# Optimization experiments

Measured on AMD Instinct MI355X. Metric: run time of the kernel, lower is better.

The kernel has to match this reference:

```python
import jax, jax.numpy as jnp
import numpy as np


def _gru_layer(x, w_ih, w_hh, b_ih, b_hh):
    """PyTorch-semantics GRU over x:[B,T,I]. w_ih:[3H,I], w_hh:[3H,H]."""
    B, T, I = x.shape
    H = w_hh.shape[1]
    # precompute input-side gates for all timesteps: [T,B,3H]
    gx = (jnp.einsum('bti,gi->btg', x, w_ih) + b_ih).transpose(1, 0, 2)

    def step(h, gx_t):
        gh = h @ w_hh.T + b_hh  # [B,3H]
        xr, xz, xn = jnp.split(gx_t, 3, axis=-1)
        hr, hz, hn = jnp.split(gh, 3, axis=-1)
        r = jax.nn.sigmoid(xr + hr)
        z = jax.nn.sigmoid(xz + hz)
        n = jnp.tanh(xn + r * hn)
        h_new = (1.0 - z) * n + z * h
        return h_new, h_new

    h0 = jnp.zeros((B, H), dtype=x.dtype)
    _, hs = jax.lax.scan(step, h0, gx)  # hs: [T,B,H]
    return hs.transpose(1, 0, 2)


def _gru_params(key, in_size, hidden):
    k = 1.0 / np.sqrt(hidden)
    k1, k2, k3, k4 = jax.random.split(key, 4)
    w_ih = jax.random.uniform(k1, (3 * hidden, in_size), minval=-k, maxval=k, dtype=jnp.float32)
    w_hh = jax.random.uniform(k2, (3 * hidden, hidden), minval=-k, maxval=k, dtype=jnp.float32)
    b_ih = jax.random.uniform(k3, (3 * hidden,), minval=-k, maxval=k, dtype=jnp.float32)
    b_hh = jax.random.uniform(k4, (3 * hidden,), minval=-k, maxval=k, dtype=jnp.float32)
    return w_ih, w_hh, b_ih, b_hh


def setup_inputs() -> dict:
    key = jax.random.key(0)
    ks = jax.random.split(key, 6)
    B, T = 256, 1024
    x = jax.random.normal(ks[0], (B, T), dtype=jnp.float32)
    sizes = [(1, 256), (256, 128), (128, 128), (128, 256)]
    d = {'x': x}
    for i, (isz, h) in enumerate(sizes):
        w_ih, w_hh, b_ih, b_hh = _gru_params(ks[1 + i], isz, h)
        d[f'w_ih{i+1}'] = w_ih
        d[f'w_hh{i+1}'] = w_hh
        d[f'b_ih{i+1}'] = b_ih
        d[f'b_hh{i+1}'] = b_hh
    kw, kb = jax.random.split(ks[5])
    kk = 1.0 / np.sqrt(256.0)
    d['w_out'] = jax.random.uniform(kw, (1, 256), minval=-kk, maxval=kk, dtype=jnp.float32)
    d['b_out'] = jax.random.uniform(kb, (1,), minval=-kk, maxval=kk, dtype=jnp.float32)
    return d


def reference(x, w_ih1, w_hh1, b_ih1, b_hh1,
              w_ih2, w_hh2, b_ih2, b_hh2,
              w_ih3, w_hh3, b_ih3, b_hh3,
              w_ih4, w_hh4, b_ih4, b_hh4,
              w_out, b_out):
    h = x[..., None]  # [B,T,1]
    h = _gru_layer(h, w_ih1, w_hh1, b_ih1, b_hh1)
    h = _gru_layer(h, w_ih2, w_hh2, b_ih2, b_hh2)
    h = _gru_layer(h, w_ih3, w_hh3, b_ih3, b_hh3)
    h = _gru_layer(h, w_ih4, w_hh4, b_ih4, b_hh4)
    y = jnp.einsum('bth,oh->bto', h, w_out) + b_out  # TimeDistributed Linear(256,1)
    return y.reshape(y.shape[0], -1)  # flatten from dim 1 -> [B,T]
```

## Files before the change

kernel.cpp:

```cpp
#include <hip/hip_runtime.h>
#include <math.h>


__device__ __forceinline__ float sigmoidf_(float v) {
    return 1.0f / (1.0f + __expf(-v));
}

__global__ void prep_k(const float* __restrict__ src, float* __restrict__ dst,
                       int H, int J) {
    int idx = blockIdx.x * 256 + threadIdx.x;
    int total = 3 * H * J;
    if (idx < total) {
        int g = idx / (H * J);
        int rem = idx - g * H * J;
        int u = rem / J;
        int j = rem - u * J;
        dst[(u * 3 + g) * J + j] = src[(g * H + u) * J + j];
    }
}


__device__ __forceinline__ void flag_st(int* p, int v) {
    __hip_atomic_store(p, v, __ATOMIC_RELAXED, __HIP_MEMORY_SCOPE_AGENT);
}
__device__ __forceinline__ int flag_ld(const int* p) {
    return __hip_atomic_load(p, __ATOMIC_RELAXED, __HIP_MEMORY_SCOPE_AGENT);
}
__device__ __forceinline__ void ex_store(float* p, float v) {
    __hip_atomic_store(p, v, __ATOMIC_RELAXED, __HIP_MEMORY_SCOPE_AGENT);
}

__device__ __forceinline__ void pollwait(const int* p, int tgt, bool active) {
    if (threadIdx.x < 64) {
        int spins = 0;
        while (true) {
            int v = active ? flag_ld(p) : 0x7fffffff;
            if (__all(v >= tgt)) break;
            if (++spins > 200000) break;
            __builtin_amdgcn_s_sleep(1);
        }
    }
    __syncthreads();
}

template <int J>
__device__ __forceinline__ void stageX(float* dst, const float* src) {
    constexpr int NF4 = (32 * J) / 1024;
    constexpr int LJ = (J == 256) ? 8 : 7;
    float4 tmp[NF4];
    #pragma unroll
    for (int k = 0; k < NF4; ++k) {
        const float* p = src + (size_t)(k * 256 + threadIdx.x) * 4;
        asm volatile("global_load_dwordx4 %0, %1, off sc0 sc1"
                     : "=v"(tmp[k]) : "v"(p) : "memory");
    }
    asm volatile("s_waitcnt vmcnt(0)" ::: "memory");
    #pragma unroll
    for (int k = 0; k < NF4; ++k) {
        int i = (k * 256 + threadIdx.x) * 4;
        int b = i >> LJ;
        int j = i & (J - 1);
        *(float4*)(dst + b * (J + 4) + j) = tmp[k];
    }
}

template <int J>
__device__ __forceinline__ void zero32(float* dst) {
    for (int i = threadIdx.x; i < 32 * (J + 4); i += 256) dst[i] = 0.0f;
}

template <int KB, int J>
__device__ __forceinline__ void dot3(const float* __restrict__ w3,
                                     const float* __restrict__ hst, int b0,
                                     float* ar, float* az, float* ac) {
    const float4* wr = (const float4*)w3;
    const float4* wz = (const float4*)(w3 + J);
    const float4* wn = (const float4*)(w3 + 2 * J);
    const float* rows[KB];
    #pragma unroll
    for (int k = 0; k < KB; ++k) rows[k] = hst + (b0 + k * (32 / KB)) * (J + 4);
    #pragma unroll 4
    for (int j4 = 0; j4 < J / 4; ++j4) {
        float4 a = wr[j4];
        float4 c = wz[j4];
        float4 d = wn[j4];
        #pragma unroll
        for (int k = 0; k < KB; ++k) {
            float4 hv = *(const float4*)(rows[k] + j4 * 4);
            ar[k] = fmaf(hv.x, a.x, ar[k]); ar[k] = fmaf(hv.y, a.y, ar[k]);
            ar[k] = fmaf(hv.z, a.z, ar[k]); ar[k] = fmaf(hv.w, a.w, ar[k]);
            az[k] = fmaf(hv.x, c.x, az[k]); az[k] = fmaf(hv.y, c.y, az[k]);
            az[k] = fmaf(hv.z, c.z, az[k]); az[k] = fmaf(hv.w, c.w, az[k]);
            ac[k] = fmaf(hv.x, d.x, ac[k]); ac[k] = fmaf(hv.y, d.y, ac[k]);
            ac[k] = fmaf(hv.z, d.z, ac[k]); ac[k] = fmaf(hv.w, d.w, ac[k]);
        }
    }
}

__global__ __launch_bounds__(256) void gru_pipe_kernel(
    const float* __restrict__ x,
    const float* __restrict__ w_ih1,
    const float* __restrict__ b_ih1, const float* __restrict__ b_hh1,
    const float* __restrict__ b_ih2, const float* __restrict__ b_hh2,
    const float* __restrict__ b_ih3, const float* __restrict__ b_hh3,
    const float* __restrict__ b_ih4, const float* __restrict__ b_hh4,
    const float* __restrict__ wA_hh1,
    const float* __restrict__ wA_ih2,
    const float* __restrict__ wA_hh2,
    const float* __restrict__ wA_ih3,
    const float* __restrict__ wA_hh3,
    const float* __restrict__ wA_ih4,
    const float* __restrict__ wA_hh4,
    const float* __restrict__ w_out, const float* __restrict__ b_out,
    int* __restrict__ flags,
    float* __restrict__ ex,
    float* __restrict__ out)
{
    const int tid = threadIdx.x;
    extern __shared__ float smem[];
    __shared__ float xs[32];
    __shared__ float wsum[4][4][8];

    const int bg = blockIdx.x & 7;
    const int rest = blockIdx.x >> 3;
    const int s = rest >> 3;
    const int us = rest & 7;

    int* fb = flags + bg * 128;
    int* arr_own = fb + s * 32;

    const int* pT = arr_own; int dT = -1000000000; bool aT = false;
    const int* pM = arr_own; int dM = -1000000000; bool aM = false;
    if (tid < 8) {
        if (s > 0) { pT = fb + (s - 1) * 32 + tid; dT = 1; aT = true; }
        pM = arr_own + tid; dM = 0; aM = true;
    } else if (tid < 16) {
        if (s < 3) { pT = fb + (s + 1) * 32 + (tid - 8); dT = -3; aT = true; }
    }

    float* exb = ex + (size_t)bg * 98304;
    float* h1r = exb;
    float* h2r = exb + 32768;
    float* h3r = exb + 49152;
    float* h4r = exb + 65536;

    if (s == 0) {
        float* wlds = smem;
        float* hprev = smem + 24704;
        {
            const float* srcw = wA_hh1 + (size_t)us * 32 * 768;
            for (int i = tid; i < 24576; i += 256) {
                int uu = i / 768, r = i - uu * 768;
                wlds[uu * 772 + r] = srcw[i];
            }
        }
        __syncthreads();
        const int ul = tid >> 3, b0 = tid & 7;
        const int u = us * 32 + ul;
        const float* wh = wlds + ul * 772;
        const float br = b_ih1[u] + b_hh1[u];
        const float bz = b_ih1[u + 256] + b_hh1[u + 256];
        const float bxn = b_ih1[u + 512];
        const float bhn = b_hh1[u + 512];
        const float wir = w_ih1[u], wiz = w_ih1[u + 256], win = w_ih1[u + 512];
        for (int t = 0; t < 1024; ++t) {
            pollwait(pT, t + dT, aT);
            if (tid < 32) xs[tid] = x[(size_t)(bg * 32 + tid) * 1024 + t];
            pollwait(pM, t + dM, aM);
            if (t > 0) stageX<256>(hprev, h1r + (size_t)((t - 1) & 3) * 8192);
            else       zero32<256>(hprev);
            __syncthreads();
            float ar[4], az[4], axn[4], ahn[4];
            #pragma unroll
            for (int k = 0; k < 4; ++k) {
                float xv = xs[b0 + 8 * k];
                ar[k] = br + xv * wir; az[k] = bz + xv * wiz;
                axn[k] = bxn + xv * win; ahn[k] = bhn;
            }
            dot3<4, 256>(wh, hprev, b0, ar, az, ahn);
            float* hout = h1r + (size_t)(t & 3) * 8192;
            #pragma unroll
            for (int k = 0; k < 4; ++k) {
                int b = b0 + 8 * k;
                float hp = hprev[b * 260 + u];
                float r = sigmoidf_(ar[k]);
                float z = sigmoidf_(az[k]);
                float n = tanhf(axn[k] + r * ahn[k]);
                ex_store(hout + b * 256 + u, (1.f - z) * n + z * hp);
            }
            asm volatile("s_waitcnt vmcnt(0)" ::: "memory");
            __syncthreads();
            if (tid == 0) flag_st(arr_own + us, t + 1);
        }
    } else if (s == 1) {
        float* wlds = smem;
        float* hin = smem + 6208;
        float* hprev = smem + 14528;
        {
            const float* srcw = wA_hh2 + (size_t)us * 16 * 384;
            for (int i = tid; i < 6144; i += 256) {
                int uu = i / 384, r = i - uu * 384;
                wlds[uu * 388 + r] = srcw[i];
            }
        }
        __syncthreads();
        const int ul = tid >> 4, b0 = tid & 15;
        const int u = us * 16 + ul;
        const float* wi = wA_ih2 + (size_t)u * 768;
        const float* wh = wlds + ul * 388;
        const float br = b_ih2[u] + b_hh2[u];
        const float bz = b_ih2[u + 128] + b_hh2[u + 128];
        const float bxn = b_ih2[u + 256];
        const float bhn = b_hh2[u + 256];
        for (int t = 0; t < 1024; ++t) {
            pollwait(pT, t + dT, aT);
            stageX<256>(hin, h1r + (size_t)(t & 3) * 8192);
            __syncthreads();
            float ar[2] = {br, br}, az[2] = {bz, bz};
            float axn[2] = {bxn, bxn}, ahn[2] = {bhn, bhn};
            dot3<2, 256>(wi, hin, b0, ar, az, axn);
            pollwait(pM, t + dM, aM);
            if (t > 0) stageX<128>(hprev, h2r + (size_t)((t - 1) & 3) * 4096);
            else       zero32<128>(hprev);
            __syncthreads();
            dot3<2, 128>(wh, hprev, b0, ar, az, ahn);
            float* hout = h2r + (size_t)(t & 3) * 4096;
            #pragma unroll
            for (int k = 0; k < 2; ++k) {
                int b = b0 + 16 * k;
                float hp = hprev[b * 132 + u];
                float r = sigmoidf_(ar[k]);
                float z = sigmoidf_(az[k]);
                float n = tanhf(axn[k] + r * ahn[k]);
                ex_store(hout + b * 128 + u, (1.f - z) * n + z * hp);
            }
            asm volatile("s_waitcnt vmcnt(0)" ::: "memory");
            __syncthreads();
            if (tid == 0) flag_st(arr_own + us, t + 1);
        }
    } else if (s == 2) {
        float* wlds = smem;
        float* hin = smem + 6208;
        float* hprev = smem + 10432;
        {
            const float* srcw = wA_hh3 + (size_t)us * 16 * 384;
            for (int i = tid; i < 6144; i += 256) {
                int uu = i / 384, r = i - uu * 384;
                wlds[uu * 388 + r] = srcw[i];
            }
        }
        __syncthreads();
        const int ul = tid >> 4, b0 = tid & 15;
        const int u = us * 16 + ul;
        const float* wi = wA_ih3 + (size_t)u * 384;
        const float* wh = wlds + ul * 388;
        const float br = b_ih3[u] + b_hh3[u];
        const float bz = b_ih3[u + 128] + b_hh3[u + 128];
        const float bxn = b_ih3[u + 256];
        const float bhn = b_hh3[u + 256];
        for (int t = 0; t < 1024; ++t) {
            pollwait(pT, t + dT, aT);
            stageX<128>(hin, h2r + (size_t)(t & 3) * 4096);
            __syncthreads();
            float ar[2] = {br, br}, az[2] = {bz, bz};
            float axn[2] = {bxn, bxn}, ahn[2] = {bhn, bhn};
            dot3<2, 128>(wi, hin, b0, ar, az, axn);
            pollwait(pM, t + dM, aM);
            if (t > 0) stageX<128>(hprev, h3r + (size_t)((t - 1) & 3) * 4096);
            else       zero32<128>(hprev);
            __syncthreads();
            dot3<2, 128>(wh, hprev, b0, ar, az, ahn);
            float* hout = h3r + (size_t)(t & 3) * 4096;
            #pragma unroll
            for (int k = 0; k < 2; ++k) {
                int b = b0 + 16 * k;
                float hp = hprev[b * 132 + u];
                float r = sigmoidf_(ar[k]);
                float z = sigmoidf_(az[k]);
                float n = tanhf(axn[k] + r * ahn[k]);
                ex_store(hout + b * 128 + u, (1.f - z) * n + z * hp);
            }
            asm volatile("s_waitcnt vmcnt(0)" ::: "memory");
            __syncthreads();
            if (tid == 0) flag_st(arr_own + us, t + 1);
        }
    } else {
        float* wlds = smem;
        float* hin = smem + 24704;
        float* hprev = smem + 28928;
        {
            const float* srcw = wA_hh4 + (size_t)us * 32 * 768;
            for (int i = tid; i < 24576; i += 256) {
                int uu = i / 768, r = i - uu * 768;
                wlds[uu * 772 + r] = srcw[i];
            }
        }
        __syncthreads();
        const int ul = tid >> 3, b0 = tid & 7;
        const int u = us * 32 + ul;
        const float* wi = wA_ih4 + (size_t)u * 384;
        const float* wh = wlds + ul * 772;
        const float br = b_ih4[u] + b_hh4[u];
        const float bz = b_ih4[u + 256] + b_hh4[u + 256];
        const float bxn = b_ih4[u + 512];
        const float bhn = b_hh4[u + 512];
        const float wo = w_out[u];
        for (int t = 0; t < 1024; ++t) {
            pollwait(pT, t + dT, aT);
            stageX<128>(hin, h3r + (size_t)(t & 3) * 4096);
            __syncthreads();
            float ar[4], az[4], axn[4], ahn[4];
            #pragma unroll
            for (int k = 0; k < 4; ++k) {
                ar[k] = br; az[k] = bz; axn[k] = bxn; ahn[k] = bhn;
            }
            dot3<4, 128>(wi, hin, b0, ar, az, axn);
            pollwait(pM, t + dM, aM);
            if (t > 0) stageX<256>(hprev, h4r + (size_t)((t - 1) & 3) * 8192);
            else       zero32<256>(hprev);
            __syncthreads();
            dot3<4, 256>(wh, hprev, b0, ar, az, ahn);
            float* hout = h4r + (size_t)(t & 3) * 8192;
            float pk[4];
            #pragma unroll
            for (int k = 0; k < 4; ++k) {
                int b = b0 + 8 * k;
                float hp = hprev[b * 260 + u];
                float r = sigmoidf_(ar[k]);
                float z = sigmoidf_(az[k]);
                float n = tanhf(axn[k] + r * ahn[k]);
                float hnew = (1.f - z) * n + z * hp;
                ex_store(hout + b * 256 + u, hnew);
                pk[k] = wo * hnew;
            }
            #pragma unroll
            for (int k = 0; k < 4; ++k) {
                pk[k] += __shfl_xor(pk[k], 8, 64);
                pk[k] += __shfl_xor(pk[k], 16, 64);
                pk[k] += __shfl_xor(pk[k], 32, 64);
            }
            if ((tid & 63) < 8) {
                int w = tid >> 6;
                #pragma unroll
                for (int k = 0; k < 4; ++k) wsum[w][k][tid & 7] = pk[k];
            }
            asm volatile("s_waitcnt vmcnt(0)" ::: "memory");
            __syncthreads();
            if (tid == 0) flag_st(arr_own + us, t + 1);
            if (tid < 32) {
                int k = tid >> 3, bb = tid & 7;
                float ssum = wsum[0][k][bb] + wsum[1][k][bb] +
                             wsum[2][k][bb] + wsum[3][k][bb];
                if (us == 0) ssum += b_out[0];
                atomicAdd(out + (size_t)(bg * 32 + bb + 8 * k) * 1024 + t, ssum);
            }
        }
    }
}

extern "C" void kernel_launch(void* const* d_in, const int* in_sizes, int n_in,
                              void* d_out, int out_size, void* d_ws, size_t ws_size,
                              hipStream_t stream) {
    const float* x     = (const float*)d_in[0];
    const float* w_ih1 = (const float*)d_in[1];
    const float* w_hh1 = (const float*)d_in[2];
    const float* b_ih1 = (const float*)d_in[3];
    const float* b_hh1 = (const float*)d_in[4];
    const float* w_ih2 = (const float*)d_in[5];
    const float* w_hh2 = (const float*)d_in[6];
    const float* b_ih2 = (const float*)d_in[7];
    const float* b_hh2 = (const float*)d_in[8];
    const float* w_ih3 = (const float*)d_in[9];
    const float* w_hh3 = (const float*)d_in[10];
    const float* b_ih3 = (const float*)d_in[11];
    const float* b_hh3 = (const float*)d_in[12];
    const float* w_ih4 = (const float*)d_in[13];
    const float* w_hh4 = (const float*)d_in[14];
    const float* b_ih4 = (const float*)d_in[15];
    const float* b_hh4 = (const float*)d_in[16];
    const float* w_out = (const float*)d_in[17];
    const float* b_out = (const float*)d_in[18];

    float* ws = (float*)d_ws;
    float* wA_hh1 = ws;
    float* wA_ih2 = wA_hh1 + 196608;
    float* wA_hh2 = wA_ih2 + 98304;
    float* wA_ih3 = wA_hh2 + 49152;
    float* wA_hh3 = wA_ih3 + 49152;
    float* wA_ih4 = wA_hh3 + 49152;
    float* wA_hh4 = wA_ih4 + 98304;
    float* ex     = wA_hh4 + 196608;
    int*   flags  = (int*)(ex + 786432);

    hipMemsetAsync(flags, 0, 1024 * sizeof(int), stream);
    hipMemsetAsync(d_out, 0, 256 * 1024 * sizeof(float), stream);

    prep_k<<<768, 256, 0, stream>>>(w_hh1, wA_hh1, 256, 256);
    prep_k<<<384, 256, 0, stream>>>(w_ih2, wA_ih2, 128, 256);
    prep_k<<<192, 256, 0, stream>>>(w_hh2, wA_hh2, 128, 128);
    prep_k<<<192, 256, 0, stream>>>(w_ih3, wA_ih3, 128, 128);
    prep_k<<<192, 256, 0, stream>>>(w_hh3, wA_hh3, 128, 128);
    prep_k<<<384, 256, 0, stream>>>(w_ih4, wA_ih4, 256, 128);
    prep_k<<<768, 256, 0, stream>>>(w_hh4, wA_hh4, 256, 256);

    const int dyn_lds = 37248 * (int)sizeof(float);
    (void)hipFuncSetAttribute((const void*)gru_pipe_kernel,
                              hipFuncAttributeMaxDynamicSharedMemorySize, dyn_lds);

    gru_pipe_kernel<<<256, 256, dyn_lds, stream>>>(
        x, w_ih1, b_ih1, b_hh1, b_ih2, b_hh2, b_ih3, b_hh3, b_ih4, b_hh4,
        wA_hh1, wA_ih2, wA_hh2, wA_ih3, wA_hh3, wA_ih4, wA_hh4,
        w_out, b_out, flags, ex, (float*)d_out);
}
```

Measured before the change: 18.27 ms.

## Prefetch next-step inputs, coalesce ring stores via LDS, and lighten flag polling

The persistent pipelined GRU kernel now polls flags per wavefront with cached flag values, so each wave skips the poll once the target is already met, and the trailing barrier after polling is removed. Layers 2-4 speculatively prefetch the next timestep's input hidden state into registers when the upstream flag already allows it, overlapping that load with the gate math. Each layer's output is staged in LDS and written to the global ring with coalesced stores instead of scattered per-thread stores. tanhf is replaced by an exp-based approximation. The cost is extra LDS, an extra barrier per step and more registers, and removing the barrier after polling makes the synchronisation more delicate.

After: 19.55 ms. +7.0%, slower.

```diff
diff --git a/kernel.cpp b/kernel.cpp
--- a/kernel.cpp
+++ b/kernel.cpp
@@ -4,6 +4,10 @@
 
 __device__ __forceinline__ float sigmoidf_(float v) {
     return 1.0f / (1.0f + __expf(-v));
+}
+__device__ __forceinline__ float tanhf_(float v) {
+    float e = __expf(2.0f * v);
+    return 1.0f - 2.0f / (e + 1.0f);
 }
 
 __global__ void prep_k(const float* __restrict__ src, float* __restrict__ dst,
@@ -30,43 +34,67 @@
     __hip_atomic_store(p, v, __ATOMIC_RELAXED, __HIP_MEMORY_SCOPE_AGENT);
 }
 
-__device__ __forceinline__ void pollwait(const int* p, int tgt, bool active) {
-    if (threadIdx.x < 64) {
-        int spins = 0;
-        while (true) {
-            int v = active ? flag_ld(p) : 0x7fffffff;
-            if (__all(v >= tgt)) break;
-            if (++spins > 200000) break;
-            __builtin_amdgcn_s_sleep(1);
-        }
-    }
-    __syncthreads();
-}
+__device__ __forceinline__ void pollw(const int* p, int tgt, bool active,
+                                      int& fc) {
+    bool need = active && (fc < tgt);
+    if (!__any(need)) return;
+    int spins = 0;
+    while (true) {
+        if (need) { fc = flag_ld(p); need = (fc < tgt); }
+        if (!__any(need)) return;
+        if (++spins > 16) __builtin_amdgcn_s_sleep(1);
+        if (spins > 200000) return;
+    }
+}
+
 
 template <int J>
-__device__ __forceinline__ void stageX(float* dst, const float* src) {
+__device__ __forceinline__ void stage_load(float4* r, const float* src) {
     constexpr int NF4 = (32 * J) / 1024;
-    constexpr int LJ = (J == 256) ? 8 : 7;
-    float4 tmp[NF4];
     #pragma unroll
     for (int k = 0; k < NF4; ++k) {
         const float* p = src + (size_t)(k * 256 + threadIdx.x) * 4;
         asm volatile("global_load_dwordx4 %0, %1, off sc0 sc1"
-                     : "=v"(tmp[k]) : "v"(p) : "memory");
-    }
-    asm volatile("s_waitcnt vmcnt(0)" ::: "memory");
+                     : "=v"(r[k]) : "v"(p) : "memory");
+    }
+}
+
+template <int J>
+__device__ __forceinline__ void stage_write(const float4* r, float* dst) {
+    constexpr int NF4 = (32 * J) / 1024;
+    constexpr int LJ = (J == 256) ? 8 : 7;
     #pragma unroll
     for (int k = 0; k < NF4; ++k) {
         int i = (k * 256 + threadIdx.x) * 4;
         int b = i >> LJ;
         int j = i & (J - 1);
-        *(float4*)(dst + b * (J + 4) + j) = tmp[k];
-    }
+        *(float4*)(dst + b * (J + 4) + j) = r[k];
+    }
+}
+
+template <int J>
+__device__ __forceinline__ void stageX(float* dst, const float* src) {
+    float4 tmp[(32 * J) / 1024];
+    stage_load<J>(tmp, src);
+    asm volatile("s_waitcnt vmcnt(0)" ::: "memory");
+    stage_write<J>(tmp, dst);
 }
 
 template <int J>
 __device__ __forceinline__ void zero32(float* dst) {
     for (int i = threadIdx.x; i < 32 * (J + 4); i += 256) dst[i] = 0.0f;
+}
+
+template <int U, int J>
+__device__ __forceinline__ void ring_store(float* hout, const float* hst) {
+    constexpr int LU = (U == 32) ? 5 : 4;
+    #pragma unroll
+    for (int k = 0; k < (32 * U) / 256; ++k) {
+        int i = k * 256 + threadIdx.x;
+        int b = i >> LU;
+        int c = i & (U - 1);
+        ex_store(hout + b * J + c, hst[b * (U + 4) + c]);
+    }
 }
 
 template <int KB, int J>
@@ -117,6 +145,7 @@
     float* __restrict__ out)
 {
     const int tid = threadIdx.x;
+    const int lane = tid & 63;
     extern __shared__ float smem[];
     __shared__ float xs[32];
     __shared__ float wsum[4][4][8];
@@ -129,14 +158,16 @@
     int* fb = flags + bg * 128;
     int* arr_own = fb + s * 32;
 
-    const int* pT = arr_own; int dT = -1000000000; bool aT = false;
-    const int* pM = arr_own; int dM = -1000000000; bool aM = false;
-    if (tid < 8) {
-        if (s > 0) { pT = fb + (s - 1) * 32 + tid; dT = 1; aT = true; }
-        pM = arr_own + tid; dM = 0; aM = true;
-    } else if (tid < 16) {
-        if (s < 3) { pT = fb + (s + 1) * 32 + (tid - 8); dT = -3; aT = true; }
-    }
+    const int* pT = arr_own; int dT = 0; bool aT = false;
+    const int* pM = arr_own; bool aM = false;
+    if (lane < 8) {
+        if (s > 0) { pT = fb + (s - 1) * 32 + lane; dT = 1; aT = true; }
+        pM = arr_own + lane; aM = true;
+    } else if (lane < 16) {
+        if (s < 3) { pT = fb + (s + 1) * 32 + (lane - 8); dT = -3; aT = true; }
+    }
+    const bool aUp = (s > 0) && (lane < 8);
+    int fcT = 0, fcM = 0;
 
     float* exb = ex + (size_t)bg * 98304;
     float* h1r = exb;
@@ -147,6 +178,7 @@
     if (s == 0) {
         float* wlds = smem;
         float* hprev = smem + 24704;
+        float* hst = smem + 33024;
         {
             const float* srcw = wA_hh1 + (size_t)us * 32 * 768;
             for (int i = tid; i < 24576; i += 256) {
@@ -164,9 +196,9 @@
         const float bhn = b_hh1[u + 512];
         const float wir = w_ih1[u], wiz = w_ih1[u + 256], win = w_ih1[u + 512];
         for (int t = 0; t < 1024; ++t) {
-            pollwait(pT, t + dT, aT);
+            pollw(pT, t + dT, aT, fcT);
             if (tid < 32) xs[tid] = x[(size_t)(bg * 32 + tid) * 1024 + t];
-            pollwait(pM, t + dM, aM);
+            pollw(pM, t, aM, fcM);
             if (t > 0) stageX<256>(hprev, h1r + (size_t)((t - 1) & 3) * 8192);
             else       zero32<256>(hprev);
             __syncthreads();
@@ -185,9 +217,11 @@
                 float hp = hprev[b * 260 + u];
                 float r = sigmoidf_(ar[k]);
                 float z = sigmoidf_(az[k]);
-                float n = tanhf(axn[k] + r * ahn[k]);
-                ex_store(hout + b * 256 + u, (1.f - z) * n + z * hp);
-            }
+                float n = tanhf_(axn[k] + r * ahn[k]);
+                hst[b * 36 + ul] = (1.f - z) * n + z * hp;
+            }
+            __syncthreads();
+            ring_store<32, 256>(hout + us * 32, hst);
             asm volatile("s_waitcnt vmcnt(0)" ::: "memory");
             __syncthreads();
             if (tid == 0) flag_st(arr_own + us, t + 1);
@@ -196,6 +230,7 @@
         float* wlds = smem;
         float* hin = smem + 6208;
         float* hprev = smem + 14528;
+        float* hst = smem + 18752;
         {
             const float* srcw = wA_hh2 + (size_t)us * 16 * 384;
             for (int i = tid; i < 6144; i += 256) {
@@ -212,18 +247,27 @@
         const float bz = b_ih2[u + 128] + b_hh2[u + 128];
         const float bxn = b_ih2[u + 256];
         const float bhn = b_hh2[u + 256];
+        float4 pregs[8];
+        bool pf = false;
         for (int t = 0; t < 1024; ++t) {
-            pollwait(pT, t + dT, aT);
-            stageX<256>(hin, h1r + (size_t)(t & 3) * 8192);
+            pollw(pT, t + dT, aT && (lane >= 8 || !pf), fcT);
+            if (pf) stage_write<256>(pregs, hin);
+            else    stageX<256>(hin, h1r + (size_t)(t & 3) * 8192);
             __syncthreads();
             float ar[2] = {br, br}, az[2] = {bz, bz};
             float axn[2] = {bxn, bxn}, ahn[2] = {bhn, bhn};
             dot3<2, 256>(wi, hin, b0, ar, az, axn);
-            pollwait(pM, t + dM, aM);
+            pollw(pM, t, aM, fcM);
             if (t > 0) stageX<128>(hprev, h2r + (size_t)((t - 1) & 3) * 4096);
             else       zero32<128>(hprev);
             __syncthreads();
             dot3<2, 128>(wh, hprev, b0, ar, az, ahn);
+            pf = false;
+            if (t < 1023) {
+                if (aUp && fcT < t + 2) fcT = flag_ld(pT);
+                pf = __all(!aUp || fcT >= t + 2);
+                if (pf) stage_load<256>(pregs, h1r + (size_t)((t + 1) & 3) * 8192);
+            }
             float* hout = h2r + (size_t)(t & 3) * 4096;
             #pragma unroll
             for (int k = 0; k < 2; ++k) {
@@ -231,9 +275,11 @@
                 float hp = hprev[b * 132 + u];
                 float r = sigmoidf_(ar[k]);
                 float z = sigmoidf_(az[k]);
-                float n = tanhf(axn[k] + r * ahn[k]);
-                ex_store(hout + b * 128 + u, (1.f - z) * n + z * hp);
-            }
+                float n = tanhf_(axn[k] + r * ahn[k]);
+                hst[b * 20 + ul] = (1.f - z) * n + z * hp;
+            }
+            __syncthreads();
+            ring_store<16, 128>(hout + us * 16, hst);
             asm volatile("s_waitcnt vmcnt(0)" ::: "memory");
             __syncthreads();
             if (tid == 0) flag_st(arr_own + us, t + 1);
@@ -242,6 +288,7 @@
         float* wlds = smem;
         float* hin = smem + 6208;
         float* hprev = smem + 10432;
+        float* hst = smem + 14656;
         {
             const float* srcw = wA_hh3 + (size_t)us * 16 * 384;
             for (int i = tid; i < 6144; i += 256) {
@@ -258,18 +305,27 @@
         const float bz = b_ih3[u + 128] + b_hh3[u + 128];
         const float bxn = b_ih3[u + 256];
         const float bhn = b_hh3[u + 256];
+        float4 pregs[4];
+        bool pf = false;
         for (int t = 0; t < 1024; ++t) {
-            pollwait(pT, t + dT, aT);
-            stageX<128>(hin, h2r + (size_t)(t & 3) * 4096);
+            pollw(pT, t + dT, aT && (lane >= 8 || !pf), fcT);
+            if (pf) stage_write<128>(pregs, hin);
+            else    stageX<128>(hin, h2r + (size_t)(t & 3) * 4096);
             __syncthreads();
             float ar[2] = {br, br}, az[2] = {bz, bz};
             float axn[2] = {bxn, bxn}, ahn[2] = {bhn, bhn};
             dot3<2, 128>(wi, hin, b0, ar, az, axn);
-            pollwait(pM, t + dM, aM);
+            pollw(pM, t, aM, fcM);
             if (t > 0) stageX<128>(hprev, h3r + (size_t)((t - 1) & 3) * 4096);
             else       zero32<128>(hprev);
             __syncthreads();
             dot3<2, 128>(wh, hprev, b0, ar, az, ahn);
+            pf = false;
+            if (t < 1023) {
+                if (aUp && fcT < t + 2) fcT = flag_ld(pT);
+                pf = __all(!aUp || fcT >= t + 2);
+                if (pf) stage_load<128>(pregs, h2r + (size_t)((t + 1) & 3) * 4096);
+            }
             float* hout = h3r + (size_t)(t & 3) * 4096;
             #pragma unroll
             for (int k = 0; k < 2; ++k) {
@@ -277,9 +333,11 @@
                 float hp = hprev[b * 132 + u];
                 float r = sigmoidf_(ar[k]);
                 float z = sigmoidf_(az[k]);
-                float n = tanhf(axn[k] + r * ahn[k]);
-                ex_store(hout + b * 128 + u, (1.f - z) * n + z * hp);
-            }
+                float n = tanhf_(axn[k] + r * ahn[k]);
+                hst[b * 20 + ul] = (1.f - z) * n + z * hp;
+            }
+            __syncthreads();
+            ring_store<16, 128>(hout + us * 16, hst);
             asm volatile("s_waitcnt vmcnt(0)" ::: "memory");
             __syncthreads();
             if (tid == 0) flag_st(arr_own + us, t + 1);
@@ -288,6 +346,7 @@
         float* wlds = smem;
         float* hin = smem + 24704;
         float* hprev = smem + 28928;
+        float* hst = smem + 37248;
         {
             const float* srcw = wA_hh4 + (size_t)us * 32 * 768;
             for (int i = tid; i < 24576; i += 256) {
@@ -305,9 +364,12 @@
         const float bxn = b_ih4[u + 512];
         const float bhn = b_hh4[u + 512];
         const float wo = w_out[u];
+        float4 pregs[4];
+        bool pf = false;
         for (int t = 0; t < 1024; ++t) {
-            pollwait(pT, t + dT, aT);
-            stageX<128>(hin, h3r + (size_t)(t & 3) * 4096);
+            pollw(pT, t + dT, aT && !pf, fcT);
+            if (pf) stage_write<128>(pregs, hin);
+            else    stageX<128>(hin, h3r + (size_t)(t & 3) * 4096);
             __syncthreads();
             float ar[4], az[4], axn[4], ahn[4];
             #pragma unroll
@@ -315,11 +377,17 @@
                 ar[k] = br; az[k] = bz; axn[k] = bxn; ahn[k] = bhn;
             }
             dot3<4, 128>(wi, hin, b0, ar, az, axn);
-            pollwait(pM, t + dM, aM);
+            pollw(pM, t, aM, fcM);
             if (t > 0) stageX<256>(hprev, h4r + (size_t)((t - 1) & 3) * 8192);
             else       zero32<256>(hprev);
             __syncthreads();
             dot3<4, 256>(wh, hprev, b0, ar, az, ahn);
+            pf = false;
+            if (t < 1023) {
+                if (aUp && fcT < t + 2) fcT = flag_ld(pT);
+                pf = __all(!aUp || fcT >= t + 2);
+                if (pf) stage_load<128>(pregs, h3r + (size_t)((t + 1) & 3) * 4096);
+            }
             float* hout = h4r + (size_t)(t & 3) * 8192;
             float pk[4];
             #pragma unroll
@@ -328,9 +396,9 @@
                 float hp = hprev[b * 260 + u];
                 float r = sigmoidf_(ar[k]);
                 float z = sigmoidf_(az[k]);
-                float n = tanhf(axn[k] + r * ahn[k]);
+                float n = tanhf_(axn[k] + r * ahn[k]);
                 float hnew = (1.f - z) * n + z * hp;
-                ex_store(hout + b * 256 + u, hnew);
+                hst[b * 36 + ul] = hnew;
                 pk[k] = wo * hnew;
             }
             #pragma unroll
@@ -344,6 +412,8 @@
                 #pragma unroll
                 for (int k = 0; k < 4; ++k) wsum[w][k][tid & 7] = pk[k];
             }
+            __syncthreads();
+            ring_store<32, 256>(hout + us * 32, hst);
             asm volatile("s_waitcnt vmcnt(0)" ::: "memory");
             __syncthreads();
             if (tid == 0) flag_st(arr_own + us, t + 1);
@@ -392,8 +462,8 @@
     float* ex     = wA_hh4 + 196608;
     int*   flags  = (int*)(ex + 786432);
 
-    hipMemsetAsync(flags, 0, 1024 * sizeof(int), stream);
-    hipMemsetAsync(d_out, 0, 256 * 1024 * sizeof(float), stream);
+    (void)hipMemsetAsync(flags, 0, 1024 * sizeof(int), stream);
+    (void)hipMemsetAsync(d_out, 0, 256 * 1024 * sizeof(float), stream);
 
     prep_k<<<768, 256, 0, stream>>>(w_hh1, wA_hh1, 256, 256);
     prep_k<<<384, 256, 0, stream>>>(w_ih2, wA_ih2, 128, 256);
@@ -403,7 +473,7 @@
     prep_k<<<384, 256, 0, stream>>>(w_ih4, wA_ih4, 256, 128);
     prep_k<<<768, 256, 0, stream>>>(w_hh4, wA_hh4, 256, 256);
 
-    const int dyn_lds = 37248 * (int)sizeof(float);
+    const int dyn_lds = 38400 * (int)sizeof(float);
     (void)hipFuncSetAttribute((const void*)gru_pipe_kernel,
                               hipFuncAttributeMaxDynamicSharedMemorySize, dyn_lds);
 
```

## Restructure GRU recurrent matvecs with per-wave batch tiles and shuffle reduce-scatter

Applied to the files above, without the earlier changes.

Each wave now stages only its own 8-batch slice of the hidden state, so the block-wide barrier before each matvec goes away. Lanes split the reduction dimension across 8 lanes and combine partial sums with a shuffle-based reduce-scatter. Results are staged in LDS and written to the ring buffer with coalesced stores. A cheaper exp-based tanh replaces tanhf, and flag polling caches the last observed value so it can skip redundant loads. The cost is more register pressure from large accumulator arrays, extra shuffle work, and a small change in tanh accuracy.

Result: slower. 19.65 ms (+7.5%).

```diff
diff --git a/kernel.cpp b/kernel.cpp
--- a/kernel.cpp
+++ b/kernel.cpp
@@ -4,6 +4,10 @@
 
 __device__ __forceinline__ float sigmoidf_(float v) {
     return 1.0f / (1.0f + __expf(-v));
+}
+__device__ __forceinline__ float tanhf_(float v) {
+    float e = __expf(2.0f * v);
+    return 1.0f - 2.0f / (e + 1.0f);
 }
 
 __global__ void prep_k(const float* __restrict__ src, float* __restrict__ dst,
@@ -30,69 +34,135 @@
     __hip_atomic_store(p, v, __ATOMIC_RELAXED, __HIP_MEMORY_SCOPE_AGENT);
 }
 
-__device__ __forceinline__ void pollwait(const int* p, int tgt, bool active) {
+__device__ __forceinline__ void pollwait(const int* p, int tgt, bool active,
+                                         int& fc) {
     if (threadIdx.x < 64) {
-        int spins = 0;
-        while (true) {
-            int v = active ? flag_ld(p) : 0x7fffffff;
-            if (__all(v >= tgt)) break;
-            if (++spins > 200000) break;
-            __builtin_amdgcn_s_sleep(1);
+        bool need = active && (fc < tgt);
+        if (__any(need)) {
+            int spins = 0;
+            while (true) {
+                if (need) { fc = flag_ld(p); need = (fc < tgt); }
+                if (!__any(need)) break;
+                if (++spins > 200000) break;
+                __builtin_amdgcn_s_sleep(1);
+            }
         }
     }
     __syncthreads();
 }
 
+
 template <int J>
-__device__ __forceinline__ void stageX(float* dst, const float* src) {
-    constexpr int NF4 = (32 * J) / 1024;
-    constexpr int LJ = (J == 256) ? 8 : 7;
+__device__ __forceinline__ void stageW(float* dst, const float* src) {
+    constexpr int NF4 = J / 32;
+    const int lane = threadIdx.x & 63;
     float4 tmp[NF4];
     #pragma unroll
     for (int k = 0; k < NF4; ++k) {
-        const float* p = src + (size_t)(k * 256 + threadIdx.x) * 4;
+        const float* p = src + (size_t)(k * 64 + lane) * 4;
         asm volatile("global_load_dwordx4 %0, %1, off sc0 sc1"
                      : "=v"(tmp[k]) : "v"(p) : "memory");
     }
     asm volatile("s_waitcnt vmcnt(0)" ::: "memory");
     #pragma unroll
-    for (int k = 0; k < NF4; ++k) {
-        int i = (k * 256 + threadIdx.x) * 4;
-        int b = i >> LJ;
-        int j = i & (J - 1);
-        *(float4*)(dst + b * (J + 4) + j) = tmp[k];
-    }
+    for (int k = 0; k < NF4; ++k)
+        *(float4*)(dst + (k * 64 + lane) * 4) = tmp[k];
 }
 
 template <int J>
-__device__ __forceinline__ void zero32(float* dst) {
-    for (int i = threadIdx.x; i < 32 * (J + 4); i += 256) dst[i] = 0.0f;
-}
-
-template <int KB, int J>
-__device__ __forceinline__ void dot3(const float* __restrict__ w3,
-                                     const float* __restrict__ hst, int b0,
-                                     float* ar, float* az, float* ac) {
-    const float4* wr = (const float4*)w3;
-    const float4* wz = (const float4*)(w3 + J);
-    const float4* wn = (const float4*)(w3 + 2 * J);
-    const float* rows[KB];
+__device__ __forceinline__ void zeroW(float* dst) {
+    const int lane = threadIdx.x & 63;
     #pragma unroll
-    for (int k = 0; k < KB; ++k) rows[k] = hst + (b0 + k * (32 / KB)) * (J + 4);
-    #pragma unroll 4
-    for (int j4 = 0; j4 < J / 4; ++j4) {
-        float4 a = wr[j4];
-        float4 c = wz[j4];
-        float4 d = wn[j4];
+    for (int k = 0; k < J / 32; ++k)
+        *(float4*)(dst + (k * 64 + lane) * 4) = make_float4(0.f, 0.f, 0.f, 0.f);
+}
+
+template <int U, int J>
+__device__ __forceinline__ void ring_store(float* hout, const float* hst) {
+    constexpr int LU = (U == 32) ? 5 : 4;
+    #pragma unroll
+    for (int k = 0; k < (32 * U) / 256; ++k) {
+        int i = k * 256 + threadIdx.x;
+        int b = i >> LU;
+        int c = i & (U - 1);
+        ex_store(hout + b * J + c, hst[b * (U + 4) + c]);
+    }
+}
+
+
+template <int J, int WST>
+__device__ __forceinline__ void dotA4(const float* __restrict__ wb,
+                                      const float* __restrict__ hb, int kl,
+                                      float (&a)[8][12]) {
+    #pragma unroll 2
+    for (int it = 0; it < J / 32; ++it) {
+        const int j = (it * 8 + kl) * 4;
+        float4 h4[8];
         #pragma unroll
-        for (int k = 0; k < KB; ++k) {
-            float4 hv = *(const float4*)(rows[k] + j4 * 4);
-            ar[k] = fmaf(hv.x, a.x, ar[k]); ar[k] = fmaf(hv.y, a.y, ar[k]);
-            ar[k] = fmaf(hv.z, a.z, ar[k]); ar[k] = fmaf(hv.w, a.w, ar[k]);
-            az[k] = fmaf(hv.x, c.x, az[k]); az[k] = fmaf(hv.y, c.y, az[k]);
-            az[k] = fmaf(hv.z, c.z, az[k]); az[k] = fmaf(hv.w, c.w, az[k]);
-            ac[k] = fmaf(hv.x, d.x, ac[k]); ac[k] = fmaf(hv.y, d.y, ac[k]);
-            ac[k] = fmaf(hv.z, d.z, ac[k]); ac[k] = fmaf(hv.w, d.w, ac[k]);
+        for (int b = 0; b < 8; ++b)
+            h4[b] = *(const float4*)(hb + b * J + j);
+        #pragma unroll
+        for (int i = 0; i < 4; ++i) {
+            #pragma unroll
+            for (int ch = 0; ch < 3; ++ch) {
+                float4 w = *(const float4*)(wb + i * WST + ch * J + j);
+                #pragma unroll
+                for (int b8 = 0; b8 < 8; ++b8) {
+                    float& acc = a[i * 2 + (b8 >> 2)][ch * 4 + (b8 & 3)];
+                    acc = fmaf(w.x, h4[b8].x, acc);
+                    acc = fmaf(w.y, h4[b8].y, acc);
+                    acc = fmaf(w.z, h4[b8].z, acc);
+                    acc = fmaf(w.w, h4[b8].w, acc);
+                }
+            }
+        }
+    }
+}
+
+template <int J, int WST>
+__device__ __forceinline__ void dotB2(const float* __restrict__ wb,
+                                      const float* __restrict__ hb, int kl,
+                                      float (&a)[8][6]) {
+    #pragma unroll 2
+    for (int it = 0; it < J / 32; ++it) {
+        const int j = (it * 8 + kl) * 4;
+        float4 h4[8];
+        #pragma unroll
+        for (int b = 0; b < 8; ++b)
+            h4[b] = *(const float4*)(hb + b * J + j);
+        #pragma unroll
+        for (int i = 0; i < 2; ++i) {
+            #pragma unroll
+            for (int ch = 0; ch < 3; ++ch) {
+                float4 w = *(const float4*)(wb + i * WST + ch * J + j);
+                #pragma unroll
+                for (int b8 = 0; b8 < 8; ++b8) {
+                    float& acc = a[i * 4 + (b8 >> 1)][ch * 2 + (b8 & 1)];
+                    acc = fmaf(w.x, h4[b8].x, acc);
+                    acc = fmaf(w.y, h4[b8].y, acc);
+                    acc = fmaf(w.z, h4[b8].z, acc);
+                    acc = fmaf(w.w, h4[b8].w, acc);
+                }
+            }
+        }
+    }
+}
+
+template <int G, int F>
+__device__ __forceinline__ void rscat(float (&a)[G][F], int kl) {
+    #pragma unroll
+    for (int lev = 0; (1 << lev) < G; ++lev) {
+        const int m = 1 << lev;
+        const int g = G >> (lev + 1);
+        const bool hi = ((kl >> lev) & 1) != 0;
+        #pragma unroll
+        for (int gg = 0; gg < g; ++gg) {
+            #pragma unroll
+            for (int f = 0; f < F; ++f) {
+                float give = hi ? a[gg][f] : a[gg + g][f];
+                float got = __shfl_xor(give, m, 64);
+                a[gg][f] = (hi ? a[gg + g][f] : a[gg][f]) + got;
+            }
         }
     }
 }
@@ -117,9 +187,13 @@
     float* __restrict__ out)
 {
     const int tid = threadIdx.x;
+    const int lane = tid & 63;
+    const int w = tid >> 6;
+    const int usl = lane >> 3;
+    const int kl = lane & 7;
+    const int gf = ((kl & 1) << 2) | (kl & 2) | ((kl >> 2) & 1);
     extern __shared__ float smem[];
     __shared__ float xs[32];
-    __shared__ float wsum[4][4][8];
 
     const int bg = blockIdx.x & 7;
     const int rest = blockIdx.x >> 3;
@@ -130,13 +204,14 @@
     int* arr_own = fb + s * 32;
 
     const int* pT = arr_own; int dT = -1000000000; bool aT = false;
-    const int* pM = arr_own; int dM = -1000000000; bool aM = false;
+    const int* pM = arr_own; bool aM = false;
     if (tid < 8) {
         if (s > 0) { pT = fb + (s - 1) * 32 + tid; dT = 1; aT = true; }
-        pM = arr_own + tid; dM = 0; aM = true;
+        pM = arr_own + tid; aM = true;
     } else if (tid < 16) {
         if (s < 3) { pT = fb + (s + 1) * 32 + (tid - 8); dT = -3; aT = true; }
     }
+    int fcT = 0, fcM = 0;
 
     float* exb = ex + (size_t)bg * 98304;
     float* h1r = exb;
@@ -147,6 +222,7 @@
     if (s == 0) {
         float* wlds = smem;
         float* hprev = smem + 24704;
+        float* hst = smem + 32896;
         {
             const float* srcw = wA_hh1 + (size_t)us * 32 * 768;
             for (int i = tid; i < 24576; i += 256) {
@@ -155,39 +231,39 @@
             }
         }
         __syncthreads();
-        const int ul = tid >> 3, b0 = tid & 7;
-        const int u = us * 32 + ul;
-        const float* wh = wlds + ul * 772;
+        const int u_sl = usl * 4 + (gf >> 1);
+        const int bhi = gf & 1;
+        const int u = us * 32 + u_sl;
+        const float* wbh = wlds + usl * 4 * 772;
+        const float* hbh = hprev + w * 2048;
         const float br = b_ih1[u] + b_hh1[u];
         const float bz = b_ih1[u + 256] + b_hh1[u + 256];
         const float bxn = b_ih1[u + 512];
         const float bhn = b_hh1[u + 512];
         const float wir = w_ih1[u], wiz = w_ih1[u + 256], win = w_ih1[u + 512];
         for (int t = 0; t < 1024; ++t) {
-            pollwait(pT, t + dT, aT);
+            pollwait(pT, t + dT, aT, fcT);
             if (tid < 32) xs[tid] = x[(size_t)(bg * 32 + tid) * 1024 + t];
-            pollwait(pM, t + dM, aM);
-            if (t > 0) stageX<256>(hprev, h1r + (size_t)((t - 1) & 3) * 8192);
-            else       zero32<256>(hprev);
-            __syncthreads();
-            float ar[4], az[4], axn[4], ahn[4];
-            #pragma unroll
-            for (int k = 0; k < 4; ++k) {
-                float xv = xs[b0 + 8 * k];
-                ar[k] = br + xv * wir; az[k] = bz + xv * wiz;
-                axn[k] = bxn + xv * win; ahn[k] = bhn;
-            }
-            dot3<4, 256>(wh, hprev, b0, ar, az, ahn);
+            pollwait(pM, t, aM, fcM);
+            if (t > 0) stageW<256>(hprev + w * 2048,
+                                   h1r + (size_t)((t - 1) & 3) * 8192 + w * 2048);
+            else       zeroW<256>(hprev + w * 2048);
+            float ah[8][12] = {};
+            dotA4<256, 772>(wbh, hbh, kl, ah);
+            rscat<8, 12>(ah, kl);
             float* hout = h1r + (size_t)(t & 3) * 8192;
             #pragma unroll
-            for (int k = 0; k < 4; ++k) {
-                int b = b0 + 8 * k;
-                float hp = hprev[b * 260 + u];
-                float r = sigmoidf_(ar[k]);
-                float z = sigmoidf_(az[k]);
-                float n = tanhf(axn[k] + r * ahn[k]);
-                ex_store(hout + b * 256 + u, (1.f - z) * n + z * hp);
-            }
+            for (int bl = 0; bl < 4; ++bl) {
+                int b32 = w * 8 + bhi * 4 + bl;
+                float xv = xs[b32];
+                float rr = sigmoidf_(ah[0][bl] + br + xv * wir);
+                float zz = sigmoidf_(ah[0][4 + bl] + bz + xv * wiz);
+                float nn = tanhf_(xv * win + bxn + rr * (ah[0][8 + bl] + bhn));
+                float hp = hprev[b32 * 256 + u];
+                hst[b32 * 36 + u_sl] = (1.f - zz) * nn + zz * hp;
+            }
+            __syncthreads();
+            ring_store<32, 256>(hout + us * 32, hst);
             asm volatile("s_waitcnt vmcnt(0)" ::: "memory");
             __syncthreads();
             if (tid == 0) flag_st(arr_own + us, t + 1);
@@ -195,7 +271,8 @@
     } else if (s == 1) {
         float* wlds = smem;
         float* hin = smem + 6208;
-        float* hprev = smem + 14528;
+        float* hprev = smem + 14400;
+        float* hst = smem + 18496;
         {
             const float* srcw = wA_hh2 + (size_t)us * 16 * 384;
             for (int i = tid; i < 6144; i += 256) {
@@ -204,36 +281,42 @@
             }
         }
         __syncthreads();
-        const int ul = tid >> 4, b0 = tid & 15;
-        const int u = us * 16 + ul;
-        const float* wi = wA_ih2 + (size_t)u * 768;
-        const float* wh = wlds + ul * 388;
+        const int u_sl = usl * 2 + (gf >> 2);
+        const int bq = gf & 3;
+        const int u = us * 16 + u_sl;
+        const float* wbh = wlds + usl * 2 * 388;
+        const float* wbi = wA_ih2 + (size_t)(us * 16 + usl * 2) * 768;
+        const float* hbi = hin + w * 2048;
+        const float* hbh = hprev + w * 1024;
         const float br = b_ih2[u] + b_hh2[u];
         const float bz = b_ih2[u + 128] + b_hh2[u + 128];
         const float bxn = b_ih2[u + 256];
         const float bhn = b_hh2[u + 256];
         for (int t = 0; t < 1024; ++t) {
-            pollwait(pT, t + dT, aT);
-            stageX<256>(hin, h1r + (size_t)(t & 3) * 8192);
-            __syncthreads();
-            float ar[2] = {br, br}, az[2] = {bz, bz};
-            float axn[2] = {bxn, bxn}, ahn[2] = {bhn, bhn};
-            dot3<2, 256>(wi, hin, b0, ar, az, axn);
-            pollwait(pM, t + dM, aM);
-            if (t > 0) stageX<128>(hprev, h2r + (size_t)((t - 1) & 3) * 4096);
-            else       zero32<128>(hprev);
-            __syncthreads();
-            dot3<2, 128>(wh, hprev, b0, ar, az, ahn);
+            pollwait(pT, t + dT, aT, fcT);
+            stageW<256>(hin + w * 2048, h1r + (size_t)(t & 3) * 8192 + w * 2048);
+            float ai[8][6] = {};
+            dotB2<256, 768>(wbi, hbi, kl, ai);
+            rscat<8, 6>(ai, kl);
+            pollwait(pM, t, aM, fcM);
+            if (t > 0) stageW<128>(hprev + w * 1024,
+                                   h2r + (size_t)((t - 1) & 3) * 4096 + w * 1024);
+            else       zeroW<128>(hprev + w * 1024);
+            float ah[8][6] = {};
+            dotB2<128, 388>(wbh, hbh, kl, ah);
+            rscat<8, 6>(ah, kl);
             float* hout = h2r + (size_t)(t & 3) * 4096;
             #pragma unroll
-            for (int k = 0; k < 2; ++k) {
-                int b = b0 + 16 * k;
-                float hp = hprev[b * 132 + u];
-                float r = sigmoidf_(ar[k]);
-                float z = sigmoidf_(az[k]);
-                float n = tanhf(axn[k] + r * ahn[k]);
-                ex_store(hout + b * 128 + u, (1.f - z) * n + z * hp);
-            }
+            for (int bl = 0; bl < 2; ++bl) {
+                int b32 = w * 8 + bq * 2 + bl;
+                float rr = sigmoidf_(ai[0][bl] + ah[0][bl] + br);
+                float zz = sigmoidf_(ai[0][2 + bl] + ah[0][2 + bl] + bz);
+                float nn = tanhf_(ai[0][4 + bl] + bxn + rr * (ah[0][4 + bl] + bhn));
+                float hp = hprev[b32 * 128 + u];
+                hst[b32 * 20 + u_sl] = (1.f - zz) * nn + zz * hp;
+            }
+            __syncthreads();
+            ring_store<16, 128>(hout + us * 16, hst);
             asm volatile("s_waitcnt vmcnt(0)" ::: "memory");
             __syncthreads();
             if (tid == 0) flag_st(arr_own + us, t + 1);
@@ -241,7 +324,8 @@
     } else if (s == 2) {
         float* wlds = smem;
         float* hin = smem + 6208;
-        float* hprev = smem + 10432;
+        float* hprev = smem + 10304;
+        float* hst = smem + 14400;
         {
             const float* srcw = wA_hh3 + (size_t)us * 16 * 384;
             for (int i = tid; i < 6144; i += 256) {
@@ -250,36 +334,42 @@
             }
         }
         __syncthreads();
-        const int ul = tid >> 4, b0 = tid & 15;
-        const int u = us * 16 + ul;
-        const float* wi = wA_ih3 + (size_t)u * 384;
-        const float* wh = wlds + ul * 388;
+        const int u_sl = usl * 2 + (gf >> 2);
+        const int bq = gf & 3;
+        const int u = us * 16 + u_sl;
+        const float* wbh = wlds + usl * 2 * 388;
+        const float* wbi = wA_ih3 + (size_t)(us * 16 + usl * 2) * 384;
+        const float* hbi = hin + w * 1024;
+        const float* hbh = hprev + w * 1024;
         const float br = b_ih3[u] + b_hh3[u];
         const float bz = b_ih3[u + 128] + b_hh3[u + 128];
         const float bxn = b_ih3[u + 256];
         const float bhn = b_hh3[u + 256];
         for (int t = 0; t < 1024; ++t) {
-            pollwait(pT, t + dT, aT);
-            stageX<128>(hin, h2r + (size_t)(t & 3) * 4096);
-            __syncthreads();
-            float ar[2] = {br, br}, az[2] = {bz, bz};
-            float axn[2] = {bxn, bxn}, ahn[2] = {bhn, bhn};
-            dot3<2, 128>(wi, hin, b0, ar, az, axn);
-            pollwait(pM, t + dM, aM);
-            if (t > 0) stageX<128>(hprev, h3r + (size_t)((t - 1) & 3) * 4096);
-            else       zero32<128>(hprev);
-            __syncthreads();
-            dot3<2, 128>(wh, hprev, b0, ar, az, ahn);
+            pollwait(pT, t + dT, aT, fcT);
+            stageW<128>(hin + w * 1024, h2r + (size_t)(t & 3) * 4096 + w * 1024);
+            float ai[8][6] = {};
+            dotB2<128, 384>(wbi, hbi, kl, ai);
+            rscat<8, 6>(ai, kl);
+            pollwait(pM, t, aM, fcM);
+            if (t > 0) stageW<128>(hprev + w * 1024,
+                                   h3r + (size_t)((t - 1) & 3) * 4096 + w * 1024);
+            else       zeroW<128>(hprev + w * 1024);
+            float ah[8][6] = {};
+            dotB2<128, 388>(wbh, hbh, kl, ah);
+            rscat<8, 6>(ah, kl);
             float* hout = h3r + (size_t)(t & 3) * 4096;
             #pragma unroll
-            for (int k = 0; k < 2; ++k) {
-                int b = b0 + 16 * k;
-                float hp = hprev[b * 132 + u];
-                float r = sigmoidf_(ar[k]);
-                float z = sigmoidf_(az[k]);
-                float n = tanhf(axn[k] + r * ahn[k]);
-                ex_store(hout + b * 128 + u, (1.f - z) * n + z * hp);
-            }
+            for (int bl = 0; bl < 2; ++bl) {
+                int b32 = w * 8 + bq * 2 + bl;
+                float rr = sigmoidf_(ai[0][bl] + ah[0][bl] + br);
+                float zz = sigmoidf_(ai[0][2 + bl] + ah[0][2 + bl] + bz);
+                float nn = tanhf_(ai[0][4 + bl] + bxn + rr * (ah[0][4 + bl] + bhn));
+                float hp = hprev[b32 * 128 + u];
+                hst[b32 * 20 + u_sl] = (1.f - zz) * nn + zz * hp;
+            }
+            __syncthreads();
+            ring_store<16, 128>(hout + us * 16, hst);
             asm volatile("s_waitcnt vmcnt(0)" ::: "memory");
             __syncthreads();
             if (tid == 0) flag_st(arr_own + us, t + 1);
@@ -287,7 +377,8 @@
     } else {
         float* wlds = smem;
         float* hin = smem + 24704;
-        float* hprev = smem + 28928;
+        float* hprev = smem + 28800;
+        float* hst = smem + 36992;
         {
             const float* srcw = wA_hh4 + (size_t)us * 32 * 768;
             for (int i = tid; i < 24576; i += 256) {
@@ -296,63 +387,64 @@
             }
         }
         __syncthreads();
-        const int ul = tid >> 3, b0 = tid & 7;
-        const int u = us * 32 + ul;
-        const float* wi = wA_ih4 + (size_t)u * 384;
-        const float* wh = wlds + ul * 772;
+        const int u_sl = usl * 4 + (gf >> 1);
+        const int bhi = gf & 1;
+        const int u = us * 32 + u_sl;
+        const float* wbh = wlds + usl * 4 * 772;
+        const float* wbi = wA_ih4 + (size_t)(us * 32 + usl * 4) * 384;
+        const float* hbi = hin + w * 1024;
+        const float* hbh = hprev + w * 2048;
         const float br = b_ih4[u] + b_hh4[u];
         const float bz = b_ih4[u + 256] + b_hh4[u + 256];
         const float bxn = b_ih4[u + 512];
         const float bhn = b_hh4[u + 512];
         const float wo = w_out[u];
         for (int t = 0; t < 1024; ++t) {
-            pollwait(pT, t + dT, aT);
-            stageX<128>(hin, h3r + (size_t)(t & 3) * 4096);
-            __syncthreads();
-            float ar[4], az[4], axn[4], ahn[4];
-            #pragma unroll
-            for (int k = 0; k < 4; ++k) {
-                ar[k] = br; az[k] = bz; axn[k] = bxn; ahn[k] = bhn;
-            }
-            dot3<4, 128>(wi, hin, b0, ar, az, axn);
-            pollwait(pM, t + dM, aM);
-            if (t > 0) stageX<256>(hprev, h4r + (size_t)((t - 1) & 3) * 8192);
-            else       zero32<256>(hprev);
-            __syncthreads();
-            dot3<4, 256>(wh, hprev, b0, ar, az, ahn);
+            pollwait(pT, t + dT, aT, fcT);
+            stageW<128>(hin + w * 1024, h3r + (size_t)(t & 3) * 4096 + w * 1024);
+            float ai[8][12] = {};
+            dotA4<128, 384>(wbi, hbi, kl, ai);
+            rscat<8, 12>(ai, kl);
+            pollwait(pM, t, aM, fcM);
+            if (t > 0) stageW<256>(hprev + w * 2048,
+                                   h4r + (size_t)((t - 1) & 3) * 8192 + w * 2048);
+            else       zeroW<256>(hprev + w * 2048);
+            float ah[8][12] = {};
+            dotA4<256, 772>(wbh, hbh, kl, ah);
+            rscat<8, 12>(ah, kl);
             float* hout = h4r + (size_t)(t & 3) * 8192;
             float pk[4];
             #pragma unroll
-            for (int k = 0; k < 4; ++k) {
-                int b = b0 + 8 * k;
-                float hp = hprev[b * 260 + u];
-                float r = sigmoidf_(ar[k]);
-                float z = sigmoidf_(az[k]);
-                float n = tanhf(axn[k] + r * ahn[k]);
-                float hnew = (1.f - z) * n + z * hp;
-                ex_store(hout + b * 256 + u, hnew);
-                pk[k] = wo * hnew;
-            }
-            #pragma unroll
-            for (int k = 0; k < 4; ++k) {
-                pk[k] += __shfl_xor(pk[k], 8, 64);
-                pk[k] += __shfl_xor(pk[k], 16, 64);
-                pk[k] += __shfl_xor(pk[k], 32, 64);
-            }
-            if ((tid & 63) < 8) {
-                int w = tid >> 6;
+            for (int bl = 0; bl < 4; ++bl) {
+                int b32 = w * 8 + bhi * 4 + bl;
+                float rr = sigmoidf_(ai[0][bl] + ah[0][bl] + br);
+                float zz = sigmoidf_(ai[0][4 + bl] + ah[0][4 + bl] + bz);
+                float nn = tanhf_(ai[0][8 + bl] + bxn + rr * (ah[0][8 + bl] + bhn));
+                float hp = hprev[b32 * 256 + u];
+                float hnew = (1.f - zz) * nn + zz * hp;
+                hst[b32 * 36 + u_sl] = hnew;
+                pk[bl] = wo * hnew;
+            }
+            #pragma unroll
+            for (int bl = 0; bl < 4; ++bl) {
+                pk[bl] += __shfl_xor(pk[bl], 1, 64);
+                pk[bl] += __shfl_xor(pk[bl], 2, 64);
+                pk[bl] += __shfl_xor(pk[bl], 8, 64);
+                pk[bl] += __shfl_xor(pk[bl], 16, 64);
+                pk[bl] += __shfl_xor(pk[bl], 32, 64);
+            }
+            __syncthreads();
+            ring_store<32, 256>(hout + us * 32, hst);
+            asm volatile("s_waitcnt vmcnt(0)" ::: "memory");
+            __syncthreads();
+            if (tid == 0) flag_st(arr_own + us, t + 1);
+            if ((lane & 59) == 0) {
                 #pragma unroll
-                for (int k = 0; k < 4; ++k) wsum[w][k][tid & 7] = pk[k];
-            }
-            asm volatile("s_waitcnt vmcnt(0)" ::: "memory");
-            __syncthreads();
-            if (tid == 0) flag_st(arr_own + us, t + 1);
-            if (tid < 32) {
-                int k = tid >> 3, bb = tid & 7;
-                float ssum = wsum[0][k][bb] + wsum[1][k][bb] +
-                             wsum[2][k][bb] + wsum[3][k][bb];
-                if (us == 0) ssum += b_out[0];
-                atomicAdd(out + (size_t)(bg * 32 + bb + 8 * k) * 1024 + t, ssum);
+                for (int bl = 0; bl < 4; ++bl) {
+                    float v = pk[bl];
+                    if (us == 0) v += b_out[0];
+                    atomicAdd(out + (size_t)(bg * 32 + w * 8 + bhi * 4 + bl) * 1024 + t, v);
+                }
             }
         }
     }
@@ -392,8 +484,8 @@
     float* ex     = wA_hh4 + 196608;
     int*   flags  = (int*)(ex + 786432);
 
-    hipMemsetAsync(flags, 0, 1024 * sizeof(int), stream);
-    hipMemsetAsync(d_out, 0, 256 * 1024 * sizeof(float), stream);
+    (void)hipMemsetAsync(flags, 0, 1024 * sizeof(int), stream);
+    (void)hipMemsetAsync(d_out, 0, 256 * 1024 * sizeof(float), stream);
 
     prep_k<<<768, 256, 0, stream>>>(w_hh1, wA_hh1, 256, 256);
     prep_k<<<384, 256, 0, stream>>>(w_ih2, wA_ih2, 128, 256);
@@ -403,7 +495,7 @@
     prep_k<<<384, 256, 0, stream>>>(w_ih4, wA_ih4, 256, 128);
     prep_k<<<768, 256, 0, stream>>>(w_hh4, wA_hh4, 256, 256);
 
-    const int dyn_lds = 37248 * (int)sizeof(float);
+    const int dyn_lds = 38144 * (int)sizeof(float);
     (void)hipFuncSetAttribute((const void*)gru_pipe_kernel,
                               hipFuncAttributeMaxDynamicSharedMemorySize, dyn_lds);
 
```
